# Performance work log

Hardware: AMD Instinct MI355X
Metric: run time of the kernel (lower is better)

Reference implementation:

```python
import jax, jax.numpy as jnp
import numpy as np

NUM_GROUPS = 8
EPS = 1e-5


def setup_inputs() -> dict:
    key = jax.random.key(0)
    k1, k2 = jax.random.split(key)
    N, C, B = 1_500_000, 64, 16
    data = jax.random.normal(k1, (N, C), dtype=jnp.float32)
    batch_id = jnp.sort(jax.random.randint(k2, (N,), 0, B, dtype=jnp.int32))
    weights = jnp.ones((1, C), dtype=jnp.float32)
    bias = jnp.zeros((1, C), dtype=jnp.float32)
    return {"data": data, "weights": weights, "bias": bias,
            "batch_id": batch_id, "batch_size": B}


def _group_broadcast(x, B, G, Cg):
    # reshape (B, C) -> (B, G, Cg), sum over Cg, broadcast back to (B, C)
    s = x.reshape(B, G, Cg).sum(-1, keepdims=True)        # (B, G, 1)
    return jnp.broadcast_to(s, (B, G, Cg)).reshape(B, G * Cg)


def reference(data, weights, bias, batch_id, batch_size):
    N, C = data.shape
    G = NUM_GROUPS
    Cg = C // G
    ones = jnp.ones((N, 1), dtype=data.dtype)
    # per-batch element count, scaled by channels-per-group (matches torch code)
    count = jax.ops.segment_sum(ones, batch_id, num_segments=batch_size) * Cg  # (B, 1)
    norm = 1.0 / (count + EPS)
    # per-(batch, group) mean
    mean = jax.ops.segment_sum(data, batch_id, num_segments=batch_size) * norm  # (B, C)
    mean = _group_broadcast(mean, batch_size, G, Cg)
    out = data - mean[batch_id]
    # per-(batch, group) variance
    var = jax.ops.segment_sum(out * out, batch_id, num_segments=batch_size) * norm
    var = _group_broadcast(var, batch_size, G, Cg)
    inv_std = 1.0 / jnp.sqrt(var + EPS)
    out = out * inv_std[batch_id]
    return out * weights + bias
```

## Files before the change

### kernel.cpp

```cpp
#include <hip/hip_runtime.h>


#define NGROUPS 8
#define CGQ     8
#define NCHAN   64
#define QPR     16
#define NB      16
#define GNEPS   1e-5f

typedef float vfloat4 __attribute__((ext_vector_type(4)));

__global__ void ogn_zero(float* __restrict__ ws) {
    int i = blockIdx.x * blockDim.x + threadIdx.x;
    if (i < 272) ws[i] = 0.f;
}

__global__ __launch_bounds__(256) void ogn_pass1(const float4* __restrict__ d4,
        const int* __restrict__ bid, float* __restrict__ ws,
        int nrows, int rows_per_blk) {
    __shared__ float lsum[NB * NGROUPS];
    __shared__ float lsq[NB * NGROUPS];
    __shared__ float lcnt[NB];
    for (int i = threadIdx.x; i < NB * NGROUPS; i += 256) { lsum[i] = 0.f; lsq[i] = 0.f; }
    if (threadIdx.x < NB) lcnt[threadIdx.x] = 0.f;
    __syncthreads();

    const int q = threadIdx.x & (QPR - 1);
    const int g = q >> 1;
    int row1 = rows_per_blk * (blockIdx.x + 1);
    if (row1 > nrows) row1 = nrows;
    int r = rows_per_blk * blockIdx.x + (threadIdx.x >> 4);

    float s = 0.f, ss = 0.f, cn = 0.f;
    int cur = -1;
    for (; r < row1; r += 16) {
        int b = bid[r];
        if (b != cur) {
            if (cur >= 0) {
                atomicAdd(&lsum[cur * NGROUPS + g], s);
                atomicAdd(&lsq[cur * NGROUPS + g], ss);
                if (q == 0) atomicAdd(&lcnt[cur], cn);
            }
            cur = b; s = 0.f; ss = 0.f; cn = 0.f;
        }
        float4 v = d4[(size_t)r * QPR + q];
        s  += (v.x + v.y) + (v.z + v.w);
        ss += (v.x * v.x + v.y * v.y) + (v.z * v.z + v.w * v.w);
        cn += 1.f;
    }
    if (cur >= 0) {
        atomicAdd(&lsum[cur * NGROUPS + g], s);
        atomicAdd(&lsq[cur * NGROUPS + g], ss);
        if (q == 0) atomicAdd(&lcnt[cur], cn);
    }
    __syncthreads();

    for (int i = threadIdx.x; i < NB * NGROUPS; i += 256) {
        float v1 = lsum[i], v2 = lsq[i];
        if (v1 != 0.f) atomicAdd(&ws[i], v1);
        if (v2 != 0.f) atomicAdd(&ws[128 + i], v2);
    }
    if (threadIdx.x < NB) {
        float v = lcnt[threadIdx.x];
        if (v != 0.f) atomicAdd(&ws[256 + threadIdx.x], v);
    }
}

__global__ void ogn_pass2(float* __restrict__ ws) {
    int i = threadIdx.x;
    if (i >= NB * NGROUPS) return;
    int b = i >> 3;
    float cnt  = ws[256 + b] * (float)CGQ;
    float norm = 1.f / (cnt + GNEPS);
    float sum  = ws[i];
    float m    = sum * norm;
    float var  = (ws[128 + i] - 2.f * m * sum + cnt * m * m) * norm;
    ws[272 + i] = m;
    ws[400 + i] = rsqrtf(var + GNEPS);
}

__global__ __launch_bounds__(256) void ogn_pass3(const float4* __restrict__ d4,
        const int* __restrict__ bid, const float4* __restrict__ w4,
        const float4* __restrict__ bia4, const float* __restrict__ ws,
        float4* __restrict__ o4, int nrows, int rows_per_blk) {
    const int q = threadIdx.x & (QPR - 1);
    const int g = q >> 1;
    const float4 wv = w4[q];
    const float4 bv = bia4[q];

    const int row0 = rows_per_blk * blockIdx.x;
    int row1 = row0 + rows_per_blk;
    if (row1 > nrows) row1 = nrows;

    int cur = -1;
    float m = 0.f, is = 0.f;
    for (int r = row1 - 1 - (int)(threadIdx.x >> 4); r >= row0; r -= 16) {
        int b = bid[r];
        if (b != cur) {
            cur = b;
            m  = ws[272 + b * NGROUPS + g];
            is = ws[400 + b * NGROUPS + g];
        }
        float4 v = d4[(size_t)r * QPR + q];
        vfloat4 o;
        o.x = (v.x - m) * is * wv.x + bv.x;
        o.y = (v.y - m) * is * wv.y + bv.y;
        o.z = (v.z - m) * is * wv.z + bv.z;
        o.w = (v.w - m) * is * wv.w + bv.w;
        __builtin_nontemporal_store(o, (vfloat4*)&o4[(size_t)r * QPR + q]);
    }
}

extern "C" void kernel_launch(void* const* d_in, const int* in_sizes, int n_in,
                              void* d_out, int out_size, void* d_ws, size_t ws_size,
                              hipStream_t stream) {
    const float* data = (const float*)d_in[0];
    const float* wts  = (const float*)d_in[1];
    const float* bias = (const float*)d_in[2];
    const int*   bid  = (const int*)d_in[3];

    const int N = in_sizes[0] / NCHAN;
    float* ws = (float*)d_ws;

    ogn_zero<<<2, 256, 0, stream>>>(ws);

    const int nblk = 2048;
    const int rpb  = (N + nblk - 1) / nblk;
    ogn_pass1<<<nblk, 256, 0, stream>>>((const float4*)data, bid, ws, N, rpb);

    ogn_pass2<<<1, 128, 0, stream>>>(ws);

    ogn_pass3<<<nblk, 256, 0, stream>>>((const float4*)data, bid,
                                        (const float4*)wts, (const float4*)bias,
                                        ws, (float4*)d_out, N, rpb);
}
```

Before: 218.9 us.

## Split passes into halves ordered for cache reuse, fold finalize into apply kernel

The stats and apply passes each run as two launches over the row halves, with the apply pass visiting the second half first. The aim is for the recently read half to still sit in the large last-level cache when it is re-read. The separate finalize kernel is removed: each apply block recomputes mean and inverse std into shared memory. Blocks whose rows share one batch id take a fast path that skips the per-row batch lookups. The cost is an extra launch and a redundant small finalize in every block.

```diff
diff --git a/kernel.cpp b/kernel.cpp
--- a/kernel.cpp
+++ b/kernel.cpp
@@ -7,6 +7,7 @@
 #define QPR     16
 #define NB      16
 #define GNEPS   1e-5f
+#define NBLK    1024
 
 typedef float vfloat4 __attribute__((ext_vector_type(4)));
 
@@ -17,120 +18,160 @@
 
 __global__ __launch_bounds__(256) void ogn_pass1(const float4* __restrict__ d4,
         const int* __restrict__ bid, float* __restrict__ ws,
-        int nrows, int rows_per_blk) {
+        int row_lo, int row_hi, int rows_per_blk) {
     __shared__ float lsum[NB * NGROUPS];
-    __shared__ float lsq[NB * NGROUPS];
+    __shared__ float lsq [NB * NGROUPS];
     __shared__ float lcnt[NB];
-    for (int i = threadIdx.x; i < NB * NGROUPS; i += 256) { lsum[i] = 0.f; lsq[i] = 0.f; }
-    if (threadIdx.x < NB) lcnt[threadIdx.x] = 0.f;
+    const int tid = threadIdx.x;
+    for (int i = tid; i < NB * NGROUPS; i += 256) { lsum[i] = 0.f; lsq[i] = 0.f; }
+    if (tid < NB) lcnt[tid] = 0.f;
     __syncthreads();
 
-    const int q = threadIdx.x & (QPR - 1);
-    const int g = q >> 1;
-    int row1 = rows_per_blk * (blockIdx.x + 1);
-    if (row1 > nrows) row1 = nrows;
-    int r = rows_per_blk * blockIdx.x + (threadIdx.x >> 4);
+    const int q        = tid & (QPR - 1);
+    const int g        = q >> 1;
+    const int lane_row = tid >> 4;
 
-    float s = 0.f, ss = 0.f, cn = 0.f;
-    int cur = -1;
-    for (; r < row1; r += 16) {
-        int b = bid[r];
-        if (b != cur) {
+    const int c0 = row_lo + rows_per_blk * blockIdx.x;
+    int c1 = c0 + rows_per_blk;
+    if (c1 > row_hi) c1 = row_hi;
+
+    if (c0 < c1) {
+        const int b0 = bid[c0];
+        if (bid[c1 - 1] == b0) {
+            float s = 0.f, ss = 0.f;
+            for (int r = c0 + lane_row; r < c1; r += 16) {
+                float4 v = d4[(size_t)r * QPR + q];
+                s  += (v.x + v.y) + (v.z + v.w);
+                ss += (v.x * v.x + v.y * v.y) + (v.z * v.z + v.w * v.w);
+            }
+            atomicAdd(&lsum[b0 * NGROUPS + g], s);
+            atomicAdd(&lsq [b0 * NGROUPS + g], ss);
+            if (q == 0) {
+                int len = c1 - c0;
+                float cn = (lane_row < len) ? (float)((len - lane_row + 15) >> 4) : 0.f;
+                if (cn != 0.f) atomicAdd(&lcnt[b0], cn);
+            }
+        } else {
+            float s = 0.f, ss = 0.f, cn = 0.f;
+            int cur = -1;
+            for (int r = c0 + lane_row; r < c1; r += 16) {
+                int b = bid[r];
+                if (b != cur) {
+                    if (cur >= 0) {
+                        atomicAdd(&lsum[cur * NGROUPS + g], s);
+                        atomicAdd(&lsq [cur * NGROUPS + g], ss);
+                        if (q == 0) atomicAdd(&lcnt[cur], cn);
+                    }
+                    cur = b; s = 0.f; ss = 0.f; cn = 0.f;
+                }
+                float4 v = d4[(size_t)r * QPR + q];
+                s  += (v.x + v.y) + (v.z + v.w);
+                ss += (v.x * v.x + v.y * v.y) + (v.z * v.z + v.w * v.w);
+                cn += 1.f;
+            }
             if (cur >= 0) {
                 atomicAdd(&lsum[cur * NGROUPS + g], s);
-                atomicAdd(&lsq[cur * NGROUPS + g], ss);
+                atomicAdd(&lsq [cur * NGROUPS + g], ss);
                 if (q == 0) atomicAdd(&lcnt[cur], cn);
             }
-            cur = b; s = 0.f; ss = 0.f; cn = 0.f;
         }
-        float4 v = d4[(size_t)r * QPR + q];
-        s  += (v.x + v.y) + (v.z + v.w);
-        ss += (v.x * v.x + v.y * v.y) + (v.z * v.z + v.w * v.w);
-        cn += 1.f;
-    }
-    if (cur >= 0) {
-        atomicAdd(&lsum[cur * NGROUPS + g], s);
-        atomicAdd(&lsq[cur * NGROUPS + g], ss);
-        if (q == 0) atomicAdd(&lcnt[cur], cn);
     }
     __syncthreads();
 
-    for (int i = threadIdx.x; i < NB * NGROUPS; i += 256) {
+    for (int i = tid; i < NB * NGROUPS; i += 256) {
         float v1 = lsum[i], v2 = lsq[i];
         if (v1 != 0.f) atomicAdd(&ws[i], v1);
         if (v2 != 0.f) atomicAdd(&ws[128 + i], v2);
     }
-    if (threadIdx.x < NB) {
-        float v = lcnt[threadIdx.x];
-        if (v != 0.f) atomicAdd(&ws[256 + threadIdx.x], v);
+    if (tid < NB) {
+        float v = lcnt[tid];
+        if (v != 0.f) atomicAdd(&ws[256 + tid], v);
     }
-}
-
-__global__ void ogn_pass2(float* __restrict__ ws) {
-    int i = threadIdx.x;
-    if (i >= NB * NGROUPS) return;
-    int b = i >> 3;
-    float cnt  = ws[256 + b] * (float)CGQ;
-    float norm = 1.f / (cnt + GNEPS);
-    float sum  = ws[i];
-    float m    = sum * norm;
-    float var  = (ws[128 + i] - 2.f * m * sum + cnt * m * m) * norm;
-    ws[272 + i] = m;
-    ws[400 + i] = rsqrtf(var + GNEPS);
 }
 
 __global__ __launch_bounds__(256) void ogn_pass3(const float4* __restrict__ d4,
         const int* __restrict__ bid, const float4* __restrict__ w4,
         const float4* __restrict__ bia4, const float* __restrict__ ws,
-        float4* __restrict__ o4, int nrows, int rows_per_blk) {
-    const int q = threadIdx.x & (QPR - 1);
-    const int g = q >> 1;
+        float4* __restrict__ o4, int row_lo, int row_hi, int rows_per_blk) {
+    __shared__ float lmean[NB * NGROUPS];
+    __shared__ float listd[NB * NGROUPS];
+    const int tid = threadIdx.x;
+    if (tid < NB * NGROUPS) {
+        int b = tid >> 3;
+        float cnt  = ws[256 + b] * (float)CGQ;
+        float sum  = ws[tid];
+        float sq   = ws[128 + tid];
+        float norm = 1.f / (cnt + GNEPS);
+        float m    = sum * norm;
+        float var  = (sq - 2.f * m * sum + cnt * m * m) * norm;
+        lmean[tid] = m;
+        listd[tid] = rsqrtf(var + GNEPS);
+    }
+    __syncthreads();
+
+    const int q        = tid & (QPR - 1);
+    const int g        = q >> 1;
+    const int lane_row = tid >> 4;
     const float4 wv = w4[q];
     const float4 bv = bia4[q];
 
-    const int row0 = rows_per_blk * blockIdx.x;
-    int row1 = row0 + rows_per_blk;
-    if (row1 > nrows) row1 = nrows;
+    const int c0 = row_lo + rows_per_blk * blockIdx.x;
+    int c1 = c0 + rows_per_blk;
+    if (c1 > row_hi) c1 = row_hi;
+    if (c0 >= c1) return;
 
-    int cur = -1;
-    float m = 0.f, is = 0.f;
-    for (int r = row1 - 1 - (int)(threadIdx.x >> 4); r >= row0; r -= 16) {
-        int b = bid[r];
-        if (b != cur) {
-            cur = b;
-            m  = ws[272 + b * NGROUPS + g];
-            is = ws[400 + b * NGROUPS + g];
+    const int b0 = bid[c0];
+    if (bid[c1 - 1] == b0) {
+        const float m  = lmean[b0 * NGROUPS + g];
+        const float is = listd[b0 * NGROUPS + g];
+        for (int r = c1 - 1 - lane_row; r >= c0; r -= 16) {
+            float4 v = d4[(size_t)r * QPR + q];
+            vfloat4 o;
+            o.x = (v.x - m) * is * wv.x + bv.x;
+            o.y = (v.y - m) * is * wv.y + bv.y;
+            o.z = (v.z - m) * is * wv.z + bv.z;
+            o.w = (v.w - m) * is * wv.w + bv.w;
+            __builtin_nontemporal_store(o, (vfloat4*)&o4[(size_t)r * QPR + q]);
         }
-        float4 v = d4[(size_t)r * QPR + q];
-        vfloat4 o;
-        o.x = (v.x - m) * is * wv.x + bv.x;
-        o.y = (v.y - m) * is * wv.y + bv.y;
-        o.z = (v.z - m) * is * wv.z + bv.z;
-        o.w = (v.w - m) * is * wv.w + bv.w;
-        __builtin_nontemporal_store(o, (vfloat4*)&o4[(size_t)r * QPR + q]);
+    } else {
+        int cur = -1; float m = 0.f, is = 0.f;
+        for (int r = c1 - 1 - lane_row; r >= c0; r -= 16) {
+            int b = bid[r];
+            if (b != cur) {
+                cur = b;
+                m  = lmean[b * NGROUPS + g];
+                is = listd[b * NGROUPS + g];
+            }
+            float4 v = d4[(size_t)r * QPR + q];
+            vfloat4 o;
+            o.x = (v.x - m) * is * wv.x + bv.x;
+            o.y = (v.y - m) * is * wv.y + bv.y;
+            o.z = (v.z - m) * is * wv.z + bv.z;
+            o.w = (v.w - m) * is * wv.w + bv.w;
+            __builtin_nontemporal_store(o, (vfloat4*)&o4[(size_t)r * QPR + q]);
+        }
     }
 }
 
 extern "C" void kernel_launch(void* const* d_in, const int* in_sizes, int n_in,
                               void* d_out, int out_size, void* d_ws, size_t ws_size,
                               hipStream_t stream) {
-    const float* data = (const float*)d_in[0];
-    const float* wts  = (const float*)d_in[1];
-    const float* bias = (const float*)d_in[2];
-    const int*   bid  = (const int*)d_in[3];
+    const float4* d4   = (const float4*)d_in[0];
+    const float4* w4   = (const float4*)d_in[1];
+    const float4* bia4 = (const float4*)d_in[2];
+    const int*    bid  = (const int*)d_in[3];
 
     const int N = in_sizes[0] / NCHAN;
-    float* ws = (float*)d_ws;
+    float* ws  = (float*)d_ws;
+    float4* o4 = (float4*)d_out;
+
+    const int mid  = N / 2;
+    const int rpbA = (mid + NBLK - 1) / NBLK;
+    const int rpbB = ((N - mid) + NBLK - 1) / NBLK;
 
     ogn_zero<<<2, 256, 0, stream>>>(ws);
-
-    const int nblk = 2048;
-    const int rpb  = (N + nblk - 1) / nblk;
-    ogn_pass1<<<nblk, 256, 0, stream>>>((const float4*)data, bid, ws, N, rpb);
-
-    ogn_pass2<<<1, 128, 0, stream>>>(ws);
-
-    ogn_pass3<<<nblk, 256, 0, stream>>>((const float4*)data, bid,
-                                        (const float4*)wts, (const float4*)bias,
-                                        ws, (float4*)d_out, N, rpb);
+    ogn_pass1<<<NBLK, 256, 0, stream>>>(d4, bid, ws, 0,   mid, rpbA);
+    ogn_pass1<<<NBLK, 256, 0, stream>>>(d4, bid, ws, mid, N,   rpbB);
+    ogn_pass3<<<NBLK, 256, 0, stream>>>(d4, bid, w4, bia4, ws, o4, mid, N,   rpbB);
+    ogn_pass3<<<NBLK, 256, 0, stream>>>(d4, bid, w4, bia4, ws, o4, 0,   mid, rpbA);
 }
```

New measurement: 265.9 us. +21.5%, slower.
